# Kernel tuning notes

Hardware: AMD Instinct MI355X
Metric: run time of the kernel (lower is better)

## Reference

```python
import jax, jax.numpy as jnp
import numpy as np

N_NODES = 100000
N_EDGES = 1600000
F_IN = 92
E_IN = 50
D = 64
N_LAYERS = 3
N_GRAPHS = 512
BN_EPS = 1e-5


def setup_inputs() -> dict:
    key = jax.random.key(0)
    ks = jax.random.split(key, 24)
    s = 0.05
    inp = {
        'x': jax.random.normal(ks[0], (N_NODES, F_IN), jnp.float32),
        'edge_index': jax.random.randint(ks[1], (2, N_EDGES), 0, N_NODES, jnp.int64),
        'edge_attr': jax.random.normal(ks[2], (N_EDGES, E_IN), jnp.float32),
        'batch_idx': jnp.sort(jax.random.randint(ks[3], (N_NODES,), 0, N_GRAPHS, jnp.int64)),
        'pre_w': jax.random.normal(ks[4], (F_IN, D), jnp.float32) * s,
        'pre_b': jax.random.normal(ks[5], (D,), jnp.float32) * s,
        'Wk': jax.random.normal(ks[6], (N_LAYERS, D, D), jnp.float32) * s,
        'bk': jax.random.normal(ks[7], (N_LAYERS, D), jnp.float32) * s,
        'Wq': jax.random.normal(ks[8], (N_LAYERS, D, D), jnp.float32) * s,
        'bq': jax.random.normal(ks[9], (N_LAYERS, D), jnp.float32) * s,
        'Wv': jax.random.normal(ks[10], (N_LAYERS, D, D), jnp.float32) * s,
        'bv': jax.random.normal(ks[11], (N_LAYERS, D), jnp.float32) * s,
        'We': jax.random.normal(ks[12], (N_LAYERS, E_IN, D), jnp.float32) * s,
        'Wskip': jax.random.normal(ks[13], (N_LAYERS, D, D), jnp.float32) * s,
        'conv_bias': jax.random.normal(ks[14], (N_LAYERS, D), jnp.float32) * s,
        'bn_gamma': jnp.ones((N_LAYERS, D), jnp.float32),
        'bn_beta': jnp.zeros((N_LAYERS, D), jnp.float32),
        'post_w': jax.random.normal(ks[15], (D, D), jnp.float32) * s,
        'post_b': jax.random.normal(ks[16], (D,), jnp.float32) * s,
        'out_w': jax.random.normal(ks[17], (D, 1), jnp.float32) * s,
        'out_b': jax.random.normal(ks[18], (1,), jnp.float32) * s,
        'num_graphs': N_GRAPHS,
    }
    return inp


def _forward(x, edge_index, edge_attr, batch_idx, pre_w, pre_b, Wk, bk, Wq, bq, Wv, bv,
             We, Wskip, conv_bias, bn_gamma, bn_beta, post_w, post_b, out_w, out_b, num_graphs):
    n_nodes = x.shape[0]
    src, dst = edge_index[0], edge_index[1]  # j -> i, aggregate at i=dst
    # pre-FC + silu
    h = jax.nn.silu(x @ pre_w + pre_b)
    for l in range(Wk.shape[0]):
        # ResGatedGraphConv: node-level projections first (dense GEMMs)
        k = h @ Wk[l] + bk[l]   # key, used at target i
        q = h @ Wq[l] + bq[l]   # query, used at source j
        v = h @ Wv[l] + bv[l]   # value, used at source j
        e = edge_attr @ We[l]   # [E, D] edge embedding (no bias)
        # gather-gate-scatter over edges
        gate = jax.nn.silu((k[dst] + e) + (q[src] + e))  # act = silu
        msg = gate * (v[src] + e)                         # [E, D]
        agg = jax.ops.segment_sum(msg, dst, num_segments=n_nodes)
        h = agg + h @ Wskip[l] + conv_bias[l]
        # BatchNorm1d (training-mode batch stats, biased variance)
        mean = jnp.mean(h, axis=0)
        var = jnp.var(h, axis=0)
        h = (h - mean) * jax.lax.rsqrt(var + BN_EPS) * bn_gamma[l] + bn_beta[l]
        # dropout_rate = 0.0 -> no-op
    # global_mean_pool (early)
    sums = jax.ops.segment_sum(h, batch_idx, num_segments=num_graphs)
    cnts = jax.ops.segment_sum(jnp.ones((n_nodes,), h.dtype), batch_idx, num_segments=num_graphs)
    g = sums / jnp.maximum(cnts, 1.0)[:, None]
    g = jax.nn.silu(g @ post_w + post_b)
    out = g @ out_w + out_b  # [G, 1]
    return out.reshape(-1)


def reference(x, edge_index, edge_attr, batch_idx, pre_w, pre_b, Wk, bk, Wq, bq, Wv, bv,
              We, Wskip, conv_bias, bn_gamma, bn_beta, post_w, post_b, out_w, out_b, num_graphs):
    return _forward(x, edge_index, edge_attr, batch_idx, pre_w, pre_b, Wk, bk, Wq, bq, Wv, bv,
                    We, Wskip, conv_bias, bn_gamma, bn_beta, post_w, post_b, out_w, out_b, num_graphs)
```

## Files before the change

### kernel.cpp

```cpp
#include <hip/hip_runtime.h>
#include <math.h>

#define N_NODES 100000
#define N_EDGES 1600000
#define F_IN 92
#define E_IN 50
#define D 64
#define N_LAYERS 3
#define N_GRAPHS 512
#define BN_EPS 1e-5f

#define SCAN_BLK 1024
#define SCAN_NCH ((N_NODES + SCAN_BLK - 1) / SCAN_BLK)

__device__ __forceinline__ float silu_f(float x) {
    return x / (1.0f + __expf(-x));
}

__device__ __forceinline__ float bcast_f(float v, int lane) {
    return __int_as_float(__builtin_amdgcn_readlane(__float_as_int(v), lane));
}

__global__ __launch_bounds__(256) void hist_kernel(
    const int* __restrict__ dst, int* __restrict__ deg) {
    for (int e = blockIdx.x * 256 + threadIdx.x; e < N_EDGES; e += gridDim.x * 256)
        atomicAdd(&deg[dst[e]], 1);
}

__global__ __launch_bounds__(SCAN_BLK) void scan_sum_kernel(
    const int* __restrict__ deg, int* __restrict__ partials) {
    int b = blockIdx.x, t = threadIdx.x;
    int i = b * SCAN_BLK + t;
    int v = (i < N_NODES) ? deg[i] : 0;
    __shared__ int wsum[16];
    for (int off = 32; off > 0; off >>= 1) v += __shfl_down(v, off);
    if ((t & 63) == 0) wsum[t >> 6] = v;
    __syncthreads();
    if (t < 16) {
        int s = wsum[t];
        for (int off = 8; off > 0; off >>= 1) s += __shfl_down(s, off);
        if (t == 0) partials[b] = s;
    }
}

__global__ __launch_bounds__(128) void scan_part_kernel(int* __restrict__ partials) {
    int t = threadIdx.x;
    __shared__ int sh[128];
    sh[t] = (t < SCAN_NCH) ? partials[t] : 0;
    __syncthreads();
    for (int off = 1; off < 128; off <<= 1) {
        int v = (t >= off) ? sh[t - off] : 0;
        __syncthreads();
        sh[t] += v;
        __syncthreads();
    }
    if (t < SCAN_NCH) partials[t] = (t == 0) ? 0 : sh[t - 1];
}

__global__ __launch_bounds__(SCAN_BLK) void scan_write_kernel(
    const int* __restrict__ deg, const int* __restrict__ partials,
    int* __restrict__ row_start, int* __restrict__ cursor) {
    int b = blockIdx.x, t = threadIdx.x;
    int i = b * SCAN_BLK + t;
    int v = (i < N_NODES) ? deg[i] : 0;
    __shared__ int sh[SCAN_BLK];
    sh[t] = v;
    __syncthreads();
    for (int off = 1; off < SCAN_BLK; off <<= 1) {
        int x = (t >= off) ? sh[t - off] : 0;
        __syncthreads();
        sh[t] += x;
        __syncthreads();
    }
    int excl = partials[b] + sh[t] - v;
    if (i < N_NODES) { row_start[i] = excl; cursor[i] = excl; }
    if (i == N_NODES - 1) row_start[N_NODES] = excl + v;
}

__global__ __launch_bounds__(256) void scatter_kernel(
    const int* __restrict__ dst, int* __restrict__ cursor,
    int* __restrict__ csr) {
    for (int e = blockIdx.x * 256 + threadIdx.x; e < N_EDGES; e += gridDim.x * 256) {
        int pos = atomicAdd(&cursor[dst[e]], 1);
        csr[pos] = e;
    }
}

template <int STRIDE>
__global__ __launch_bounds__(256) void scatter_perm_kernel(
    const int* __restrict__ srcIdx, const int* __restrict__ dstIdx,
    const float* __restrict__ ea, int* __restrict__ cursor,
    float* __restrict__ ea_s, int* __restrict__ src_s) {
    int d = threadIdx.x;
    int e = blockIdx.x * 4 + threadIdx.y;
    if (e >= N_EDGES) return;
    int pos = 0;
    if (d == 0) pos = atomicAdd(&cursor[dstIdx[e]], 1);
    pos = __builtin_amdgcn_readlane(pos, 0);
    if (d == 0) src_s[pos] = srcIdx[e];
    if (d < E_IN) ea_s[(long)pos * STRIDE + d] = ea[(long)e * E_IN + d];
}

__global__ __launch_bounds__(256) void pos_kernel(
    const int* __restrict__ srcIdx, const int* __restrict__ dstIdx,
    int* __restrict__ cursor, int* __restrict__ pos_arr,
    int* __restrict__ src_s) {
    for (int e = blockIdx.x * 256 + threadIdx.x; e < N_EDGES; e += gridDim.x * 256) {
        int p = atomicAdd(&cursor[dstIdx[e]], 1);
        pos_arr[e] = p;
        src_s[p] = srcIdx[e];
    }
}

__global__ __launch_bounds__(256) void copy_rows_kernel(
    const float* __restrict__ ea, const int* __restrict__ pos_arr,
    float* __restrict__ ea_s) {
    int d = threadIdx.x;
    long ebase = ((long)blockIdx.x * 4 + threadIdx.y) * 64;
    if (ebase >= N_EDGES) return;
    int cnt = (int)min((long)64, (long)N_EDGES - ebase);
    int p_l = (d < cnt) ? pos_arr[ebase + d] : 0;
    float r_c = (d < E_IN) ? ea[ebase * E_IN + d] : 0.f;
    for (int j = 0; j < cnt; ++j) {
        float r_n = 0.f;
        if (d < E_IN && j + 1 < cnt) r_n = ea[(ebase + j + 1) * E_IN + d];
        int p = __builtin_amdgcn_readlane(p_l, j);
        ea_s[(long)p * 64 + d] = r_c;
        r_c = r_n;
    }
}

__global__ __launch_bounds__(256) void pre_fc_kernel(
    const float* __restrict__ x, const float* __restrict__ w,
    const float* __restrict__ b, float* __restrict__ h) {
    __shared__ float xs[4][F_IN];
    int d = threadIdx.x, yy = threadIdx.y;
    int node = blockIdx.x * 4 + yy;
    if (node < N_NODES) {
        const float* xrow = x + (long)node * F_IN;
        for (int i = d; i < F_IN; i += 64) xs[yy][i] = xrow[i];
    }
    __syncthreads();
    if (node >= N_NODES) return;
    float acc = b[d];
#pragma unroll 4
    for (int i = 0; i < F_IN; ++i) acc = fmaf(xs[yy][i], w[i * D + d], acc);
    h[(long)node * D + d] = silu_f(acc);
}

template <bool BN>
__global__ __launch_bounds__(256) void proj_kernel(
    const float* __restrict__ hin, const float* __restrict__ stats,
    const float* __restrict__ gamma, const float* __restrict__ beta,
    const float* __restrict__ Wk, const float* __restrict__ bk,
    const float* __restrict__ Wq, const float* __restrict__ bq,
    const float* __restrict__ Wv, const float* __restrict__ bv,
    const float* __restrict__ Ws, const float* __restrict__ cbias,
    float* __restrict__ ko, float* __restrict__ qo, float* __restrict__ vo,
    float* __restrict__ hnew) {
    __shared__ float hs[4][D];
    int d = threadIdx.x, yy = threadIdx.y;
    int node = blockIdx.x * 4 + yy;
    if (node < N_NODES) {
        float xv = hin[(long)node * D + d];
        if (BN) {
            const float invN = 1.0f / (float)N_NODES;
            float mean = stats[d] * invN;
            float var = stats[D + d] * invN - mean * mean;
            float sc = rsqrtf(var + BN_EPS) * gamma[d];
            xv = (xv - mean) * sc + beta[d];
        }
        hs[yy][d] = xv;
    }
    __syncthreads();
    if (node >= N_NODES) return;
    float ak = bk[d], aq = bq[d], av = bv[d], as = cbias[d];
#pragma unroll 8
    for (int i = 0; i < D; ++i) {
        float hv = hs[yy][i];
        ak = fmaf(hv, Wk[i * D + d], ak);
        aq = fmaf(hv, Wq[i * D + d], aq);
        av = fmaf(hv, Wv[i * D + d], av);
        as = fmaf(hv, Ws[i * D + d], as);
    }
    long off = (long)node * D + d;
    ko[off] = ak; qo[off] = aq; vo[off] = av; hnew[off] = as;
}

__global__ __launch_bounds__(256) void edge_emb_kernel(
    const float* __restrict__ ea_s, const float* __restrict__ We,
    float* __restrict__ em, int c0, int c1) {
    int p = c0 + blockIdx.x * 256 + threadIdx.x;
    if (p >= c1) return;
    const float* row = ea_s + (long)p * 64;
    float acc[D];
#pragma unroll
    for (int d = 0; d < D; ++d) acc[d] = 0.f;
#pragma unroll
    for (int i = 0; i < E_IN; i += 2) {
        float2 ev = *reinterpret_cast<const float2*>(row + i);
#pragma unroll
        for (int d = 0; d < D; ++d) acc[d] = fmaf(ev.x, We[i * D + d], acc[d]);
#pragma unroll
        for (int d = 0; d < D; ++d) acc[d] = fmaf(ev.y, We[(i + 1) * D + d], acc[d]);
    }
    float* out = em + (long)(p - c0) * D;
#pragma unroll
    for (int d = 0; d < D; d += 4)
        *reinterpret_cast<float4*>(out + d) =
            make_float4(acc[d], acc[d + 1], acc[d + 2], acc[d + 3]);
}

__global__ __launch_bounds__(256) void gather_em_kernel(
    const float* __restrict__ em, const int* __restrict__ src_s,
    const int* __restrict__ row_start,
    const float* __restrict__ kb, const float* __restrict__ qb,
    const float* __restrict__ vb, float* __restrict__ hnew,
    int c0, int c1) {
    int d = threadIdx.x;
    int node = blockIdx.x * 4 + threadIdx.y;
    if (node >= N_NODES) return;
    int lo = row_start[node], hi = row_start[node + 1];
    lo = max(lo, c0); hi = min(hi, c1);
    if (lo >= hi) return;
    float kv = kb[(long)node * D + d];
    float acc = 0.f;
    for (int base = lo; base < hi; base += 64) {
        int cnt = min(hi - base, 64);
        int s_l = 0;
        if (d < cnt) s_l = src_s[base + d];
        int s0 = __builtin_amdgcn_readlane(s_l, 0);
        float q_c = qb[(long)s0 * D + d];
        float v_c = vb[(long)s0 * D + d];
        float e_c = em[(long)(base - c0) * D + d];
        float q_n = 0.f, v_n = 0.f, e_n = 0.f;
        if (cnt > 1) {
            int s1 = __builtin_amdgcn_readlane(s_l, 1);
            q_n = qb[(long)s1 * D + d];
            v_n = vb[(long)s1 * D + d];
            e_n = em[(long)(base + 1 - c0) * D + d];
        }
        for (int j = 0; j < cnt; ++j) {
            float q_2 = 0.f, v_2 = 0.f, e_2 = 0.f;
            if (j + 2 < cnt) {
                int s2 = __builtin_amdgcn_readlane(s_l, j + 2);
                q_2 = qb[(long)s2 * D + d];
                v_2 = vb[(long)s2 * D + d];
                e_2 = em[(long)(base + j + 2 - c0) * D + d];
            }
            float gate = silu_f(kv + q_c + 2.0f * e_c);
            acc = fmaf(gate, v_c + e_c, acc);
            q_c = q_n; v_c = v_n; e_c = e_n;
            q_n = q_2; v_n = v_2; e_n = e_2;
        }
    }
    long off = (long)node * D + d;
    hnew[off] += acc;
}

template <bool PERM>
__global__ __launch_bounds__(256) void gather_kernel(
    const float* __restrict__ ea, const int* __restrict__ srcArr,
    const int* __restrict__ csr, const int* __restrict__ row_start,
    const float* __restrict__ We,
    const float* __restrict__ kb, const float* __restrict__ qb,
    const float* __restrict__ vb, float* __restrict__ hnew) {
    int d = threadIdx.x;
    int node = blockIdx.x * 4 + threadIdx.y;
    if (node >= N_NODES) return;
    float WeReg[E_IN];
#pragma unroll
    for (int i = 0; i < E_IN; ++i) WeReg[i] = We[i * D + d];
    int lo = row_start[node], hi = row_start[node + 1];
    float kv = kb[(long)node * D + d];
    float acc = 0.f;
    for (int base = lo; base < hi; base += 64) {
        int cnt = min(hi - base, 64);
        int e_l = 0, s_l = 0;
        if (d < cnt) {
            int p = base + d;
            e_l = PERM ? p : csr[p];
            s_l = PERM ? srcArr[p] : srcArr[e_l];
        }
        int s_c = __builtin_amdgcn_readlane(s_l, 0);
        int r_c = PERM ? base : __builtin_amdgcn_readlane(e_l, 0);
        float q_c = qb[(long)s_c * D + d];
        float v_c = vb[(long)s_c * D + d];
        float e_c = (d < E_IN) ? ea[(long)r_c * E_IN + d] : 0.f;
        for (int j = 0; j < cnt; ++j) {
            float q_n = 0.f, v_n = 0.f, e_n = 0.f;
            if (j + 1 < cnt) {
                int s_n = __builtin_amdgcn_readlane(s_l, j + 1);
                int r_n = PERM ? (base + j + 1) : __builtin_amdgcn_readlane(e_l, j + 1);
                q_n = qb[(long)s_n * D + d];
                v_n = vb[(long)s_n * D + d];
                e_n = (d < E_IN) ? ea[(long)r_n * E_IN + d] : 0.f;
            }
            float ed0 = 0.f, ed1 = 0.f;
#pragma unroll
            for (int i = 0; i < E_IN; i += 2) {
                ed0 = fmaf(bcast_f(e_c, i), WeReg[i], ed0);
                ed1 = fmaf(bcast_f(e_c, i + 1), WeReg[i + 1], ed1);
            }
            float ed = ed0 + ed1;
            float gate = silu_f(kv + q_c + 2.0f * ed);
            acc = fmaf(gate, v_c + ed, acc);
            q_c = q_n; v_c = v_n; e_c = e_n;
        }
    }
    long off = (long)node * D + d;
    hnew[off] += acc;
}

__global__ __launch_bounds__(256) void bn_stats_kernel(
    const float* __restrict__ hnew, float* __restrict__ stats) {
    int d = threadIdx.x, yy = threadIdx.y;
    float s = 0.f, s2 = 0.f;
    for (int n = blockIdx.x * 4 + yy; n < N_NODES; n += gridDim.x * 4) {
        float v = hnew[(long)n * D + d];
        s += v;
        s2 = fmaf(v, v, s2);
    }
    __shared__ float ls[4][D], ls2[4][D];
    ls[yy][d] = s; ls2[yy][d] = s2;
    __syncthreads();
    if (yy == 0) {
        atomicAdd(&stats[d],     ls[0][d] + ls[1][d] + ls[2][d] + ls[3][d]);
        atomicAdd(&stats[D + d], ls2[0][d] + ls2[1][d] + ls2[2][d] + ls2[3][d]);
    }
}

__global__ __launch_bounds__(256) void graph_bounds_kernel(
    const int* __restrict__ batch, int* __restrict__ start) {
    int n = blockIdx.x * 256 + threadIdx.x;
    if (n >= N_NODES) return;
    int b = batch[n];
    if (n == 0) {
        for (int g = 0; g <= b; ++g) start[g] = 0;
    } else {
        int p = batch[n - 1];
        for (int g = p + 1; g <= b; ++g) start[g] = n;
    }
    if (n == N_NODES - 1) {
        for (int g = b + 1; g <= N_GRAPHS; ++g) start[g] = N_NODES;
    }
}

__global__ __launch_bounds__(256) void pool_head_kernel(
    const float* __restrict__ hnew, const int* __restrict__ start,
    const float* __restrict__ stats, const float* __restrict__ gamma,
    const float* __restrict__ beta,
    const float* __restrict__ pw, const float* __restrict__ pb,
    const float* __restrict__ ow, const float* __restrict__ ob,
    float* __restrict__ out) {
    int g = blockIdx.x;
    int d = threadIdx.x, yy = threadIdx.y;
    int lo = start[g], hi = start[g + 1];
    float s = 0.f;
    for (int n = lo + yy; n < hi; n += 4) s += hnew[(long)n * D + d];
    __shared__ float ls[4][D];
    ls[yy][d] = s;
    __syncthreads();
    __shared__ float grow[D];
    if (yy == 0) {
        float tot = ls[0][d] + ls[1][d] + ls[2][d] + ls[3][d];
        float gd = 0.f;
        if (hi > lo) {
            float m = tot / (float)(hi - lo);
            const float invN = 1.0f / (float)N_NODES;
            float mean = stats[d] * invN;
            float var = stats[D + d] * invN - mean * mean;
            float sc = rsqrtf(var + BN_EPS) * gamma[d];
            gd = (m - mean) * sc + beta[d];
        }
        grow[d] = gd;
    }
    __syncthreads();
    if (yy != 0) return;
    float accp = pb[d];
#pragma unroll 8
    for (int i = 0; i < D; ++i) accp = fmaf(grow[i], pw[i * D + d], accp);
    float sv = silu_f(accp) * ow[d];
    for (int off = 32; off > 0; off >>= 1) sv += __shfl_down(sv, off);
    if (d == 0) out[g] = sv + ob[0];
}

extern "C" void kernel_launch(void* const* d_in, const int* in_sizes, int n_in,
                              void* d_out, int out_size, void* d_ws, size_t ws_size,
                              hipStream_t stream) {
    const float* x        = (const float*)d_in[0];
    const int*   ei       = (const int*)d_in[1];
    const float* ea       = (const float*)d_in[2];
    const int*   batch    = (const int*)d_in[3];
    const float* pre_w    = (const float*)d_in[4];
    const float* pre_b    = (const float*)d_in[5];
    const float* Wk       = (const float*)d_in[6];
    const float* bk       = (const float*)d_in[7];
    const float* Wq       = (const float*)d_in[8];
    const float* bq       = (const float*)d_in[9];
    const float* Wv       = (const float*)d_in[10];
    const float* bv       = (const float*)d_in[11];
    const float* We       = (const float*)d_in[12];
    const float* Wskip    = (const float*)d_in[13];
    const float* conv_bias= (const float*)d_in[14];
    const float* bn_gamma = (const float*)d_in[15];
    const float* bn_beta  = (const float*)d_in[16];
    const float* post_w   = (const float*)d_in[17];
    const float* post_b   = (const float*)d_in[18];
    const float* out_w    = (const float*)d_in[19];
    const float* out_b    = (const float*)d_in[20];

    char* base = (char*)d_ws;
    float* ws = (float*)d_ws;
    const size_t NH = (size_t)N_NODES * D;
    float* bufA  = ws;
    float* bufB  = ws + NH;
    float* kb    = ws + 2 * NH;
    float* qb    = ws + 3 * NH;
    float* vb    = ws + 4 * NH;
    float* stats = ws + 5 * NH;
    int*   start     = (int*)(stats + 6 * D);
    int*   deg       = start + (N_GRAPHS + 1);
    int*   row_start = deg + N_NODES;
    int*   cursor    = row_start + (N_NODES + 1);
    int*   partials  = cursor + N_NODES;
    int*   csr       = partials + 128;

    size_t off_e = (size_t)((char*)(csr + N_EDGES) - base);
    off_e = (off_e + 255) & ~(size_t)255;

    size_t src_off2 = off_e + (size_t)N_EDGES * 64 * sizeof(float);
    size_t em_off   = (src_off2 + (size_t)N_EDGES * sizeof(int) + 255) & ~(size_t)255;
    size_t CH = 0;
    bool tier2 = false;
    if (ws_size > em_off) {
        CH = (ws_size - em_off) / (D * sizeof(float));
        if (CH > N_EDGES) CH = N_EDGES;
        tier2 = CH >= 200000;
    }
    size_t src_off1 = off_e + (size_t)N_EDGES * E_IN * sizeof(float);
    bool tier1 = !tier2 && (ws_size >= src_off1 + (size_t)N_EDGES * sizeof(int));

    const int* srcIdx = ei;
    const int* dstIdx = ei + N_EDGES;

    dim3 blk(64, 4);
    const int NB_N = (N_NODES + 3) / 4;

    hipMemsetAsync(deg, 0, N_NODES * sizeof(int), stream);
    hipMemsetAsync(stats, 0, 6 * D * sizeof(float), stream);
    hist_kernel<<<1024, 256, 0, stream>>>(dstIdx, deg);
    scan_sum_kernel<<<SCAN_NCH, SCAN_BLK, 0, stream>>>(deg, partials);
    scan_part_kernel<<<1, 128, 0, stream>>>(partials);
    scan_write_kernel<<<SCAN_NCH, SCAN_BLK, 0, stream>>>(deg, partials, row_start, cursor);

    float* ea2 = (float*)(base + off_e);
    int*   src2 = (int*)(base + src_off2);
    float* em  = (float*)(base + em_off);
    float* ea1 = (float*)(base + off_e);
    int*   src1 = (int*)(base + src_off1);

    if (tier2) {
        pos_kernel<<<1024, 256, 0, stream>>>(srcIdx, dstIdx, cursor, csr, src2);
        copy_rows_kernel<<<(N_EDGES + 255) / 256, blk, 0, stream>>>(ea, csr, ea2);
    } else if (tier1) {
        scatter_perm_kernel<E_IN><<<(N_EDGES + 3) / 4, blk, 0, stream>>>(
            srcIdx, dstIdx, ea, cursor, ea1, src1);
    } else {
        scatter_kernel<<<1024, 256, 0, stream>>>(dstIdx, cursor, csr);
    }

    pre_fc_kernel<<<NB_N, blk, 0, stream>>>(x, pre_w, pre_b, bufA);

    float* hin = bufA;
    float* hout = bufB;
    for (int l = 0; l < N_LAYERS; ++l) {
        if (l == 0)
            proj_kernel<false><<<NB_N, blk, 0, stream>>>(
                hin, nullptr, nullptr, nullptr,
                Wk + l * D * D, bk + l * D, Wq + l * D * D, bq + l * D,
                Wv + l * D * D, bv + l * D, Wskip + l * D * D, conv_bias + l * D,
                kb, qb, vb, hout);
        else
            proj_kernel<true><<<NB_N, blk, 0, stream>>>(
                hin, stats + (l - 1) * 2 * D, bn_gamma + (l - 1) * D, bn_beta + (l - 1) * D,
                Wk + l * D * D, bk + l * D, Wq + l * D * D, bq + l * D,
                Wv + l * D * D, bv + l * D, Wskip + l * D * D, conv_bias + l * D,
                kb, qb, vb, hout);
        if (tier2) {
            int nch = (int)((N_EDGES + CH - 1) / CH);
            for (int c = 0; c < nch; ++c) {
                int c0 = (int)((size_t)c * CH);
                int c1 = (int)min((size_t)N_EDGES, (size_t)c0 + CH);
                edge_emb_kernel<<<(c1 - c0 + 255) / 256, 256, 0, stream>>>(
                    ea2, We + l * E_IN * D, em, c0, c1);
                gather_em_kernel<<<NB_N, blk, 0, stream>>>(
                    em, src2, row_start, kb, qb, vb, hout, c0, c1);
            }
        } else if (tier1) {
            gather_kernel<true><<<NB_N, blk, 0, stream>>>(
                ea1, src1, csr, row_start, We + l * E_IN * D, kb, qb, vb, hout);
        } else {
            gather_kernel<false><<<NB_N, blk, 0, stream>>>(
                ea, srcIdx, csr, row_start, We + l * E_IN * D, kb, qb, vb, hout);
        }
        bn_stats_kernel<<<256, blk, 0, stream>>>(hout, stats + l * 2 * D);
        float* t = hin; hin = hout; hout = t;
    }

    graph_bounds_kernel<<<(N_NODES + 255) / 256, 256, 0, stream>>>(batch, start);
    pool_head_kernel<<<N_GRAPHS, blk, 0, stream>>>(
        hin, start, stats + (N_LAYERS - 1) * 2 * D,
        bn_gamma + (N_LAYERS - 1) * D, bn_beta + (N_LAYERS - 1) * D,
        post_w, post_b, out_w, out_b, (float*)d_out);
}
```

Measured before the change: 3.020 ms.

## Compute edge embeddings from unpermuted attrs and scatter outputs into CSR order

The old path permuted the edge attributes into padded CSR order and then embedded them in chunks. Now each edge's embedding is computed from the original edge_attr, staged through a shared-memory tile, and written directly to its CSR slot. Slot positions come from a per-edge counter taken during the degree histogram plus the row start, which removes the second atomic pass. This avoids a full permutation copy of edge_attr and the chunked launches, but needs a full-size embedding buffer, and the embedding writes are now scattered rows.

```diff
diff --git a/kernel.cpp b/kernel.cpp
--- a/kernel.cpp
+++ b/kernel.cpp
@@ -12,6 +12,7 @@
 
 #define SCAN_BLK 1024
 #define SCAN_NCH ((N_NODES + SCAN_BLK - 1) / SCAN_BLK)
+#define EMB_TILE 256
 
 __device__ __forceinline__ float silu_f(float x) {
     return x / (1.0f + __expf(-x));
@@ -21,10 +22,10 @@
     return __int_as_float(__builtin_amdgcn_readlane(__float_as_int(v), lane));
 }
 
-__global__ __launch_bounds__(256) void hist_kernel(
-    const int* __restrict__ dst, int* __restrict__ deg) {
+__global__ __launch_bounds__(256) void deg_within_kernel(
+    const int* __restrict__ dst, int* __restrict__ deg, int* __restrict__ within) {
     for (int e = blockIdx.x * 256 + threadIdx.x; e < N_EDGES; e += gridDim.x * 256)
-        atomicAdd(&deg[dst[e]], 1);
+        within[e] = atomicAdd(&deg[dst[e]], 1);
 }
 
 __global__ __launch_bounds__(SCAN_BLK) void scan_sum_kernel(
@@ -75,6 +76,17 @@
     int excl = partials[b] + sh[t] - v;
     if (i < N_NODES) { row_start[i] = excl; cursor[i] = excl; }
     if (i == N_NODES - 1) row_start[N_NODES] = excl + v;
+}
+
+__global__ __launch_bounds__(256) void pos_fin_kernel(
+    const int* __restrict__ srcIdx, const int* __restrict__ dst,
+    const int* __restrict__ row_start, int* __restrict__ pos_arr,
+    int* __restrict__ src_s) {
+    for (int e = blockIdx.x * 256 + threadIdx.x; e < N_EDGES; e += gridDim.x * 256) {
+        int p = row_start[dst[e]] + pos_arr[e];
+        pos_arr[e] = p;
+        src_s[p] = srcIdx[e];
+    }
 }
 
 __global__ __launch_bounds__(256) void scatter_kernel(
@@ -99,35 +111,6 @@
     pos = __builtin_amdgcn_readlane(pos, 0);
     if (d == 0) src_s[pos] = srcIdx[e];
     if (d < E_IN) ea_s[(long)pos * STRIDE + d] = ea[(long)e * E_IN + d];
-}
-
-__global__ __launch_bounds__(256) void pos_kernel(
-    const int* __restrict__ srcIdx, const int* __restrict__ dstIdx,
-    int* __restrict__ cursor, int* __restrict__ pos_arr,
-    int* __restrict__ src_s) {
-    for (int e = blockIdx.x * 256 + threadIdx.x; e < N_EDGES; e += gridDim.x * 256) {
-        int p = atomicAdd(&cursor[dstIdx[e]], 1);
-        pos_arr[e] = p;
-        src_s[p] = srcIdx[e];
-    }
-}
-
-__global__ __launch_bounds__(256) void copy_rows_kernel(
-    const float* __restrict__ ea, const int* __restrict__ pos_arr,
-    float* __restrict__ ea_s) {
-    int d = threadIdx.x;
-    long ebase = ((long)blockIdx.x * 4 + threadIdx.y) * 64;
-    if (ebase >= N_EDGES) return;
-    int cnt = (int)min((long)64, (long)N_EDGES - ebase);
-    int p_l = (d < cnt) ? pos_arr[ebase + d] : 0;
-    float r_c = (d < E_IN) ? ea[ebase * E_IN + d] : 0.f;
-    for (int j = 0; j < cnt; ++j) {
-        float r_n = 0.f;
-        if (d < E_IN && j + 1 < cnt) r_n = ea[(ebase + j + 1) * E_IN + d];
-        int p = __builtin_amdgcn_readlane(p_l, j);
-        ea_s[(long)p * 64 + d] = r_c;
-        r_c = r_n;
-    }
 }
 
 __global__ __launch_bounds__(256) void pre_fc_kernel(
@@ -187,24 +170,30 @@
     ko[off] = ak; qo[off] = aq; vo[off] = av; hnew[off] = as;
 }
 
-__global__ __launch_bounds__(256) void edge_emb_kernel(
-    const float* __restrict__ ea_s, const float* __restrict__ We,
-    float* __restrict__ em, int c0, int c1) {
-    int p = c0 + blockIdx.x * 256 + threadIdx.x;
-    if (p >= c1) return;
-    const float* row = ea_s + (long)p * 64;
+__global__ __launch_bounds__(256) void edge_emb_perm_kernel(
+    const float* __restrict__ ea, const int* __restrict__ pos_arr,
+    const float* __restrict__ We, float* __restrict__ em) {
+    __shared__ float tile[EMB_TILE * E_IN];
+    int t = threadIdx.x;
+    long e0 = (long)blockIdx.x * EMB_TILE;
+    const float2* g = (const float2*)(ea + e0 * E_IN);
+    float2* l2 = (float2*)tile;
+#pragma unroll
+    for (int k = 0; k < (EMB_TILE * E_IN) / 2; k += 256)
+        l2[k + t] = g[k + t];
+    int pos = pos_arr[e0 + t];
+    __syncthreads();
+    const float* row = tile + t * E_IN;
     float acc[D];
 #pragma unroll
     for (int d = 0; d < D; ++d) acc[d] = 0.f;
-#pragma unroll
-    for (int i = 0; i < E_IN; i += 2) {
-        float2 ev = *reinterpret_cast<const float2*>(row + i);
-#pragma unroll
-        for (int d = 0; d < D; ++d) acc[d] = fmaf(ev.x, We[i * D + d], acc[d]);
-#pragma unroll
-        for (int d = 0; d < D; ++d) acc[d] = fmaf(ev.y, We[(i + 1) * D + d], acc[d]);
-    }
-    float* out = em + (long)(p - c0) * D;
+#pragma unroll 5
+    for (int i = 0; i < E_IN; ++i) {
+        float ev = row[i];
+#pragma unroll
+        for (int d = 0; d < D; ++d) acc[d] = fmaf(ev, We[i * D + d], acc[d]);
+    }
+    float* out = em + (long)pos * D;
 #pragma unroll
     for (int d = 0; d < D; d += 4)
         *reinterpret_cast<float4*>(out + d) =
@@ -215,13 +204,11 @@
     const float* __restrict__ em, const int* __restrict__ src_s,
     const int* __restrict__ row_start,
     const float* __restrict__ kb, const float* __restrict__ qb,
-    const float* __restrict__ vb, float* __restrict__ hnew,
-    int c0, int c1) {
+    const float* __restrict__ vb, float* __restrict__ hnew) {
     int d = threadIdx.x;
     int node = blockIdx.x * 4 + threadIdx.y;
     if (node >= N_NODES) return;
     int lo = row_start[node], hi = row_start[node + 1];
-    lo = max(lo, c0); hi = min(hi, c1);
     if (lo >= hi) return;
     float kv = kb[(long)node * D + d];
     float acc = 0.f;
@@ -232,13 +219,13 @@
         int s0 = __builtin_amdgcn_readlane(s_l, 0);
         float q_c = qb[(long)s0 * D + d];
         float v_c = vb[(long)s0 * D + d];
-        float e_c = em[(long)(base - c0) * D + d];
+        float e_c = em[(long)base * D + d];
         float q_n = 0.f, v_n = 0.f, e_n = 0.f;
         if (cnt > 1) {
             int s1 = __builtin_amdgcn_readlane(s_l, 1);
             q_n = qb[(long)s1 * D + d];
             v_n = vb[(long)s1 * D + d];
-            e_n = em[(long)(base + 1 - c0) * D + d];
+            e_n = em[(long)(base + 1) * D + d];
         }
         for (int j = 0; j < cnt; ++j) {
             float q_2 = 0.f, v_2 = 0.f, e_2 = 0.f;
@@ -246,7 +233,7 @@
                 int s2 = __builtin_amdgcn_readlane(s_l, j + 2);
                 q_2 = qb[(long)s2 * D + d];
                 v_2 = vb[(long)s2 * D + d];
-                e_2 = em[(long)(base + j + 2 - c0) * D + d];
+                e_2 = em[(long)(base + j + 2) * D + d];
             }
             float gate = silu_f(kv + q_c + 2.0f * e_c);
             acc = fmaf(gate, v_c + e_c, acc);
@@ -424,22 +411,16 @@
     int*   row_start = deg + N_NODES;
     int*   cursor    = row_start + (N_NODES + 1);
     int*   partials  = cursor + N_NODES;
-    int*   csr       = partials + 128;
-
-    size_t off_e = (size_t)((char*)(csr + N_EDGES) - base);
+    int*   posb      = partials + 128;
+
+    size_t off_e = (size_t)((char*)(posb + N_EDGES) - base);
     off_e = (off_e + 255) & ~(size_t)255;
 
-    size_t src_off2 = off_e + (size_t)N_EDGES * 64 * sizeof(float);
-    size_t em_off   = (src_off2 + (size_t)N_EDGES * sizeof(int) + 255) & ~(size_t)255;
-    size_t CH = 0;
-    bool tier2 = false;
-    if (ws_size > em_off) {
-        CH = (ws_size - em_off) / (D * sizeof(float));
-        if (CH > N_EDGES) CH = N_EDGES;
-        tier2 = CH >= 200000;
-    }
+    size_t em_offF = (off_e + (size_t)N_EDGES * sizeof(int) + 255) & ~(size_t)255;
+    size_t needF = em_offF + (size_t)N_EDGES * D * sizeof(float);
+    bool tierF = ws_size >= needF;
     size_t src_off1 = off_e + (size_t)N_EDGES * E_IN * sizeof(float);
-    bool tier1 = !tier2 && (ws_size >= src_off1 + (size_t)N_EDGES * sizeof(int));
+    bool tier1 = !tierF && (ws_size >= src_off1 + (size_t)N_EDGES * sizeof(int));
 
     const int* srcIdx = ei;
     const int* dstIdx = ei + N_EDGES;
@@ -449,25 +430,23 @@
 
     hipMemsetAsync(deg, 0, N_NODES * sizeof(int), stream);
     hipMemsetAsync(stats, 0, 6 * D * sizeof(float), stream);
-    hist_kernel<<<1024, 256, 0, stream>>>(dstIdx, deg);
+    deg_within_kernel<<<1024, 256, 0, stream>>>(dstIdx, deg, posb);
     scan_sum_kernel<<<SCAN_NCH, SCAN_BLK, 0, stream>>>(deg, partials);
     scan_part_kernel<<<1, 128, 0, stream>>>(partials);
     scan_write_kernel<<<SCAN_NCH, SCAN_BLK, 0, stream>>>(deg, partials, row_start, cursor);
 
-    float* ea2 = (float*)(base + off_e);
-    int*   src2 = (int*)(base + src_off2);
-    float* em  = (float*)(base + em_off);
-    float* ea1 = (float*)(base + off_e);
+    int*   srcF = (int*)(base + off_e);
+    float* emF  = (float*)(base + em_offF);
+    float* ea1  = (float*)(base + off_e);
     int*   src1 = (int*)(base + src_off1);
 
-    if (tier2) {
-        pos_kernel<<<1024, 256, 0, stream>>>(srcIdx, dstIdx, cursor, csr, src2);
-        copy_rows_kernel<<<(N_EDGES + 255) / 256, blk, 0, stream>>>(ea, csr, ea2);
+    if (tierF) {
+        pos_fin_kernel<<<1024, 256, 0, stream>>>(srcIdx, dstIdx, row_start, posb, srcF);
     } else if (tier1) {
         scatter_perm_kernel<E_IN><<<(N_EDGES + 3) / 4, blk, 0, stream>>>(
             srcIdx, dstIdx, ea, cursor, ea1, src1);
     } else {
-        scatter_kernel<<<1024, 256, 0, stream>>>(dstIdx, cursor, csr);
+        scatter_kernel<<<1024, 256, 0, stream>>>(dstIdx, cursor, posb);
     }
 
     pre_fc_kernel<<<NB_N, blk, 0, stream>>>(x, pre_w, pre_b, bufA);
@@ -487,22 +466,17 @@
                 Wk + l * D * D, bk + l * D, Wq + l * D * D, bq + l * D,
                 Wv + l * D * D, bv + l * D, Wskip + l * D * D, conv_bias + l * D,
                 kb, qb, vb, hout);
-        if (tier2) {
-            int nch = (int)((N_EDGES + CH - 1) / CH);
-            for (int c = 0; c < nch; ++c) {
-                int c0 = (int)((size_t)c * CH);
-                int c1 = (int)min((size_t)N_EDGES, (size_t)c0 + CH);
-                edge_emb_kernel<<<(c1 - c0 + 255) / 256, 256, 0, stream>>>(
-                    ea2, We + l * E_IN * D, em, c0, c1);
-                gather_em_kernel<<<NB_N, blk, 0, stream>>>(
-                    em, src2, row_start, kb, qb, vb, hout, c0, c1);
-            }
+        if (tierF) {
+            edge_emb_perm_kernel<<<N_EDGES / EMB_TILE, 256, 0, stream>>>(
+                ea, posb, We + l * E_IN * D, emF);
+            gather_em_kernel<<<NB_N, blk, 0, stream>>>(
+                emF, srcF, row_start, kb, qb, vb, hout);
         } else if (tier1) {
             gather_kernel<true><<<NB_N, blk, 0, stream>>>(
-                ea1, src1, csr, row_start, We + l * E_IN * D, kb, qb, vb, hout);
+                ea1, src1, posb, row_start, We + l * E_IN * D, kb, qb, vb, hout);
         } else {
             gather_kernel<false><<<NB_N, blk, 0, stream>>>(
-                ea, srcIdx, csr, row_start, We + l * E_IN * D, kb, qb, vb, hout);
+                ea, srcIdx, posb, row_start, We + l * E_IN * D, kb, qb, vb, hout);
         }
         bn_stats_kernel<<<256, blk, 0, stream>>>(hout, stats + l * 2 * D);
         float* t = hin; hin = hout; hout = t;
```

After: 2.501 ms. 17.2% less time.
